# Performance work log

Measured on AMD Instinct MI355X. Metric: run time of the kernel, lower is better.

## Reference

```python
import jax, jax.numpy as jnp
import numpy as np

B, N = 8192, 4096
OUT_DIM = 32


def setup_inputs() -> dict:
    key = jax.random.key(0)
    k_rr, k_drop, k_w1, k_b1, k_w2, k_b2 = jax.random.split(key, 6)
    rr = jax.random.uniform(k_rr, (B, N), dtype=jnp.float32, minval=0.4, maxval=1.4)
    drop = jax.random.uniform(k_drop, (B, N)) < 0.3
    rr = jnp.where(drop, 0.0, rr)
    # projection MLP params (Linear(6,16) -> ReLU -> Dropout(eval: identity) -> Linear(16,32))
    w1 = jax.random.normal(k_w1, (6, 16), dtype=jnp.float32) * (1.0 / np.sqrt(6))
    b1 = jax.random.normal(k_b1, (16,), dtype=jnp.float32) * 0.01
    w2 = jax.random.normal(k_w2, (16, OUT_DIM), dtype=jnp.float32) * (1.0 / np.sqrt(16))
    b2 = jax.random.normal(k_b2, (OUT_DIM,), dtype=jnp.float32) * 0.01
    return {"rr_intervals": rr, "w1": w1, "b1": b1, "w2": w2, "b2": b2}


def _hrv_features(rr):
    # rr: (B, N) float32, zero-padded. Faithful to the per-row torch loop, vectorized.
    dt = rr.dtype
    mask = rr > 0                                   # (B, N)
    cnt = jnp.sum(mask, axis=1)                     # (B,) int
    cntf = cnt.astype(dt)
    # masked mean / unbiased std (torch.std default ddof=1)
    denom_m = jnp.maximum(cntf, 1.0)
    mean_rr = jnp.sum(jnp.where(mask, rr, 0.0), axis=1) / denom_m
    dev = jnp.where(mask, rr - mean_rr[:, None], 0.0)
    var = jnp.sum(dev * dev, axis=1) / jnp.maximum(cntf - 1.0, 1.0)
    sdnn = jnp.sqrt(var)
    # compact valid entries to the front (stable -> preserves order), so diffs
    # match torch.diff(rr[rr > 0])
    order = jnp.argsort(jnp.logical_not(mask), axis=1, stable=True)  # (B, N)
    compact = jnp.take_along_axis(rr, order, axis=1)                  # (B, N)
    diffs = compact[:, 1:] - compact[:, :-1]                          # (B, N-1)
    dmask = jnp.arange(N - 1)[None, :] < (cnt - 1)[:, None]           # valid diffs
    ndiff = jnp.maximum(cntf - 1.0, 1.0)
    rmssd = jnp.sqrt(jnp.sum(jnp.where(dmask, diffs * diffs, 0.0), axis=1) / ndiff)
    nn50 = jnp.sum(((jnp.abs(diffs) > 0.05) & dmask).astype(dt), axis=1)
    pnn50 = nn50 / ndiff
    hr = 60.0 / jnp.maximum(mean_rr, 1e-12)
    cv = sdnn / jnp.maximum(mean_rr, 1e-12)
    feats = jnp.stack([mean_rr, sdnn, rmssd, pnn50, hr, cv], axis=1)  # (B, 6)
    feats = jnp.where((cnt > 1)[:, None], feats, 0.0)
    # per-column batch normalization, applied only where column max > 0
    col_max = jnp.max(feats, axis=0)
    col_mean = jnp.mean(feats, axis=0)
    col_std = jnp.std(feats, axis=0, ddof=1)
    normed = (feats - col_mean[None, :]) / (col_std[None, :] + 1e-8)
    feats = jnp.where((col_max > 0)[None, :], normed, feats)
    return feats


def reference(rr_intervals, w1, b1, w2, b2):
    feats = _hrv_features(rr_intervals)                 # (B, 6)
    h = jax.nn.relu(feats @ w1 + b1)                    # (B, 16); dropout in eval = identity
    return h @ w2 + b2                                  # (B, OUT_DIM)
```

## Files before the change

### kernel.cpp

```cpp
#include <hip/hip_runtime.h>
#include <math.h>

#define BATCH 8192
#define NLEN 4096

__global__ __launch_bounds__(256) void hrv_feats_kernel(
    const float* __restrict__ rr, float* __restrict__ feats) {
    const int lane = threadIdx.x & 63;
    const int wid = threadIdx.x >> 6;
    const int row = blockIdx.x * 4 + wid;
    const float* r = rr + (size_t)row * NLEN + lane * 64;

    double dsum = 0.0, dsumsq = 0.0, dsumd2 = 0.0;
    int cnt = 0, nn50 = 0, has = 0;
    float first = 0.f, last = 0.f;

    float x[32];
    float4* xv = reinterpret_cast<float4*>(x);
    const float4* rv = reinterpret_cast<const float4*>(r);

#pragma unroll
    for (int half = 0; half < 2; ++half) {
#pragma unroll
        for (int i = 0; i < 8; ++i) xv[i] = rv[half * 8 + i];
#pragma unroll
        for (int c = 0; c < 2; ++c) {
            float s = 0.f, s2 = 0.f, d2 = 0.f;
#pragma unroll
            for (int i = 0; i < 16; ++i) {
                float v = x[c * 16 + i];
                if (v > 0.f) {
                    s += v;
                    s2 += v * v;
                    ++cnt;
                    if (has) {
                        float d = v - last;
                        d2 += d * d;
                        nn50 += (fabsf(d) > 0.05f) ? 1 : 0;
                    } else {
                        first = v;
                        has = 1;
                    }
                    last = v;
                }
            }
            dsum += s;
            dsumsq += s2;
            dsumd2 += d2;
        }
    }

    unsigned long long m = __ballot(has != 0);
    unsigned long long pm = (lane == 0) ? 0ull : (m & ((1ull << lane) - 1ull));
    int j = 63 - __clzll(pm | 1ull);
    float lastj = __shfl(last, j, 64);
    if (has && pm) {
        float d = first - lastj;
        dsumd2 += (double)(d * d);
        nn50 += (fabsf(d) > 0.05f) ? 1 : 0;
    }

#pragma unroll
    for (int off = 32; off; off >>= 1) {
        dsum += __shfl_down(dsum, off, 64);
        dsumsq += __shfl_down(dsumsq, off, 64);
        dsumd2 += __shfl_down(dsumd2, off, 64);
        cnt += __shfl_down(cnt, off, 64);
        nn50 += __shfl_down(nn50, off, 64);
    }

    if (lane == 0) {
        const float cntf = (float)cnt;
        const float denom_m = fmaxf(cntf, 1.f);
        const float mean = (float)(dsum / (double)denom_m);
        const float varsum = (float)(dsumsq - (double)cnt * (double)mean * (double)mean);
        const float denom_v = fmaxf(cntf - 1.f, 1.f);
        const float sdnn = sqrtf(fmaxf(varsum / denom_v, 0.f));
        const float rmssd = sqrtf(fmaxf((float)(dsumd2 / (double)denom_v), 0.f));
        const float pnn50 = (float)nn50 / denom_v;
        const float hr = 60.f / fmaxf(mean, 1e-12f);
        const float cv = sdnn / fmaxf(mean, 1e-12f);
        float f0 = mean, f1 = sdnn, f2 = rmssd, f3 = pnn50, f4 = hr, f5 = cv;
        if (cnt <= 1) { f0 = f1 = f2 = f3 = f4 = f5 = 0.f; }
        float* o = feats + row * 6;
        o[0] = f0; o[1] = f1; o[2] = f2;
        o[3] = f3; o[4] = f4; o[5] = f5;
    }
}

__global__ __launch_bounds__(256) void stats_mlp_kernel(
    const float* __restrict__ feats,
    const float* __restrict__ w1, const float* __restrict__ b1,
    const float* __restrict__ w2, const float* __restrict__ b2,
    float* __restrict__ out) {
    __shared__ double sh_s[4][6], sh_s2[4][6];
    __shared__ float sh_m[4][6];
    __shared__ float sh_stats[18];

    const int t = threadIdx.x;
    double s[6] = {0, 0, 0, 0, 0, 0};
    double s2[6] = {0, 0, 0, 0, 0, 0};
    float mx[6] = {-INFINITY, -INFINITY, -INFINITY, -INFINITY, -INFINITY, -INFINITY};

#pragma unroll 4
    for (int i = t; i < BATCH; i += 256) {
        const float* fp = feats + i * 6;
#pragma unroll
        for (int c = 0; c < 6; ++c) {
            float f = fp[c];
            s[c] += (double)f;
            s2[c] += (double)f * (double)f;
            mx[c] = fmaxf(mx[c], f);
        }
    }
#pragma unroll
    for (int off = 32; off; off >>= 1) {
#pragma unroll
        for (int c = 0; c < 6; ++c) {
            s[c] += __shfl_down(s[c], off, 64);
            s2[c] += __shfl_down(s2[c], off, 64);
            mx[c] = fmaxf(mx[c], __shfl_down(mx[c], off, 64));
        }
    }
    if ((t & 63) == 0) {
        const int w = t >> 6;
#pragma unroll
        for (int c = 0; c < 6; ++c) {
            sh_s[w][c] = s[c];
            sh_s2[w][c] = s2[c];
            sh_m[w][c] = mx[c];
        }
    }
    __syncthreads();
    if (t < 6) {
        double S = 0, S2 = 0;
        float M = -INFINITY;
        for (int w = 0; w < 4; ++w) {
            S += sh_s[w][t];
            S2 += sh_s2[w][t];
            M = fmaxf(M, sh_m[w][t]);
        }
        const double meanb = S / (double)BATCH;
        double var = (S2 - (double)BATCH * meanb * meanb) / (double)(BATCH - 1);
        if (var < 0.0) var = 0.0;
        sh_stats[t] = (float)meanb;
        sh_stats[6 + t] = (float)sqrt(var);
        sh_stats[12 + t] = M;
    }
    __syncthreads();

    const int row = blockIdx.x * 256 + t;
    const float* fp = feats + row * 6;
    float f[6];
#pragma unroll
    for (int c = 0; c < 6; ++c) {
        float v = fp[c];
        if (sh_stats[12 + c] > 0.f) v = (v - sh_stats[c]) / (sh_stats[6 + c] + 1e-8f);
        f[c] = v;
    }
    float h[16];
#pragma unroll
    for (int j = 0; j < 16; ++j) {
        float a = b1[j];
#pragma unroll
        for (int c = 0; c < 6; ++c) a = fmaf(f[c], w1[c * 16 + j], a);
        h[j] = fmaxf(a, 0.f);
    }
    float o[32];
#pragma unroll
    for (int k = 0; k < 32; ++k) o[k] = b2[k];
#pragma unroll
    for (int j = 0; j < 16; ++j) {
        const float hj = h[j];
#pragma unroll
        for (int k = 0; k < 32; ++k) o[k] = fmaf(hj, w2[j * 32 + k], o[k]);
    }
    float4* ov = reinterpret_cast<float4*>(out + (size_t)row * 32);
    const float4* op = reinterpret_cast<const float4*>(o);
#pragma unroll
    for (int i = 0; i < 8; ++i) ov[i] = op[i];
}

extern "C" void kernel_launch(void* const* d_in, const int* in_sizes, int n_in,
                              void* d_out, int out_size, void* d_ws, size_t ws_size,
                              hipStream_t stream) {
    const float* rr = (const float*)d_in[0];
    const float* w1 = (const float*)d_in[1];
    const float* b1 = (const float*)d_in[2];
    const float* w2 = (const float*)d_in[3];
    const float* b2 = (const float*)d_in[4];
    float* out = (float*)d_out;
    float* feats = (float*)d_ws;

    hrv_feats_kernel<<<BATCH / 4, 256, 0, stream>>>(rr, feats);
    stats_mlp_kernel<<<BATCH / 256, 256, 0, stream>>>(feats, w1, b1, w2, b2, out);
}
```

Measured before the change: 41.59 us.

## Coalesce row loads with lane-interleaved float4 chunks and per-chunk ballot stitching

Each lane now reads a float4 at stride 256 floats, so a wavefront's loads cover contiguous memory instead of each lane reading its own 64-float span. Because consecutive valid elements now cross lanes at every chunk, the code does a ballot and shuffle per chunk to find the previous valid value and carries a running last value across chunks. This targets poor load coalescing on the bandwidth-bound pass over the input. In exchange it adds 16 ballot/shuffle rounds per row, which costs extra ALU and cross-lane work.

```diff
diff --git a/kernel.cpp b/kernel.cpp
--- a/kernel.cpp
+++ b/kernel.cpp
@@ -9,26 +9,29 @@
     const int lane = threadIdx.x & 63;
     const int wid = threadIdx.x >> 6;
     const int row = blockIdx.x * 4 + wid;
-    const float* r = rr + (size_t)row * NLEN + lane * 64;
+    const float* rbase = rr + (size_t)row * NLEN + lane * 4;
 
     double dsum = 0.0, dsumsq = 0.0, dsumd2 = 0.0;
-    int cnt = 0, nn50 = 0, has = 0;
-    float first = 0.f, last = 0.f;
-
-    float x[32];
-    float4* xv = reinterpret_cast<float4*>(x);
-    const float4* rv = reinterpret_cast<const float4*>(r);
+    int cnt = 0, nn50 = 0;
+    float run_last = 0.f;
+    int run_has = 0;
 
 #pragma unroll
     for (int half = 0; half < 2; ++half) {
-#pragma unroll
-        for (int i = 0; i < 8; ++i) xv[i] = rv[half * 8 + i];
-#pragma unroll
-        for (int c = 0; c < 2; ++c) {
-            float s = 0.f, s2 = 0.f, d2 = 0.f;
-#pragma unroll
-            for (int i = 0; i < 16; ++i) {
-                float v = x[c * 16 + i];
+        float4 v4[8];
+#pragma unroll
+        for (int ii = 0; ii < 8; ++ii)
+            v4[ii] = *reinterpret_cast<const float4*>(rbase + (half * 8 + ii) * 256);
+
+        float s = 0.f, s2 = 0.f, d2 = 0.f;
+#pragma unroll
+        for (int ii = 0; ii < 8; ++ii) {
+            const float x[4] = {v4[ii].x, v4[ii].y, v4[ii].z, v4[ii].w};
+            float first = 0.f, last = 0.f;
+            int has = 0;
+#pragma unroll
+            for (int k = 0; k < 4; ++k) {
+                float v = x[k];
                 if (v > 0.f) {
                     s += v;
                     s2 += v * v;
@@ -44,20 +47,26 @@
                     last = v;
                 }
             }
-            dsum += s;
-            dsumsq += s2;
-            dsumd2 += d2;
-        }
-    }
-
-    unsigned long long m = __ballot(has != 0);
-    unsigned long long pm = (lane == 0) ? 0ull : (m & ((1ull << lane) - 1ull));
-    int j = 63 - __clzll(pm | 1ull);
-    float lastj = __shfl(last, j, 64);
-    if (has && pm) {
-        float d = first - lastj;
-        dsumd2 += (double)(d * d);
-        nn50 += (fabsf(d) > 0.05f) ? 1 : 0;
+            unsigned long long m = __ballot(has != 0);
+            unsigned long long pm = m & ((1ull << lane) - 1ull);
+            int j = 63 - __clzll(pm | 1ull);
+            float lastj = __shfl(last, j, 64);
+            float pred = pm ? lastj : run_last;
+            int pred_has = pm ? 1 : run_has;
+            if (has && pred_has) {
+                float d = first - pred;
+                d2 += d * d;
+                nn50 += (fabsf(d) > 0.05f) ? 1 : 0;
+            }
+            if (m) {
+                int jm = 63 - __clzll(m);
+                run_last = __shfl(last, jm, 64);
+                run_has = 1;
+            }
+        }
+        dsum += s;
+        dsumsq += s2;
+        dsumd2 += d2;
     }
 
 #pragma unroll
```

New measurement: 42.79 us. 1.03x slower.

## Branchless HRV accumulation, column-major feature layout, vectorized stats reads

Applied to the files above, without the earlier changes.

Replaces the per-element data-dependent branches in the feature kernel with predicated selects and FMAs. This relies on invalid entries being exactly zero, so adding them to the sums changes nothing. The reduction now uses xor shuffles so every lane holds the totals, and six lanes each write one feature into a column-major (6 x BATCH) workspace. The stats kernel reads each column with float4 loads and reads the features coalesced in the MLP stage, which removes strided 6-float row accesses. The risk is extra ALU work per element where the branchy version could skip invalid values.

```diff
diff --git a/kernel.cpp b/kernel.cpp
--- a/kernel.cpp
+++ b/kernel.cpp
@@ -12,8 +12,9 @@
     const float* r = rr + (size_t)row * NLEN + lane * 64;
 
     double dsum = 0.0, dsumsq = 0.0, dsumd2 = 0.0;
-    int cnt = 0, nn50 = 0, has = 0;
-    float first = 0.f, last = 0.f;
+    int cnt = 0, nn50 = 0;
+    float prev = 0.f, first = 0.f;
+    bool has = false;
 
     float x[32];
     float4* xv = reinterpret_cast<float4*>(x);
@@ -28,21 +29,18 @@
             float s = 0.f, s2 = 0.f, d2 = 0.f;
 #pragma unroll
             for (int i = 0; i < 16; ++i) {
-                float v = x[c * 16 + i];
-                if (v > 0.f) {
-                    s += v;
-                    s2 += v * v;
-                    ++cnt;
-                    if (has) {
-                        float d = v - last;
-                        d2 += d * d;
-                        nn50 += (fabsf(d) > 0.05f) ? 1 : 0;
-                    } else {
-                        first = v;
-                        has = 1;
-                    }
-                    last = v;
-                }
+                const float v = x[c * 16 + i];
+                const bool valid = v > 0.f;
+                s += v;
+                s2 = fmaf(v, v, s2);
+                cnt += valid ? 1 : 0;
+                const float d = v - prev;
+                const float dm = (valid && has) ? d : 0.f;
+                d2 = fmaf(dm, dm, d2);
+                nn50 += (fabsf(dm) > 0.05f) ? 1 : 0;
+                first = (valid && !has) ? v : first;
+                prev = valid ? v : prev;
+                has = has || valid;
             }
             dsum += s;
             dsumsq += s2;
@@ -50,10 +48,10 @@
         }
     }
 
-    unsigned long long m = __ballot(has != 0);
-    unsigned long long pm = (lane == 0) ? 0ull : (m & ((1ull << lane) - 1ull));
+    unsigned long long m = __ballot(has);
+    unsigned long long pm = m & ((1ull << lane) - 1ull);
     int j = 63 - __clzll(pm | 1ull);
-    float lastj = __shfl(last, j, 64);
+    float lastj = __shfl(prev, j, 64);
     if (has && pm) {
         float d = first - lastj;
         dsumd2 += (double)(d * d);
@@ -62,30 +60,32 @@
 
 #pragma unroll
     for (int off = 32; off; off >>= 1) {
-        dsum += __shfl_down(dsum, off, 64);
-        dsumsq += __shfl_down(dsumsq, off, 64);
-        dsumd2 += __shfl_down(dsumd2, off, 64);
-        cnt += __shfl_down(cnt, off, 64);
-        nn50 += __shfl_down(nn50, off, 64);
-    }
-
-    if (lane == 0) {
-        const float cntf = (float)cnt;
-        const float denom_m = fmaxf(cntf, 1.f);
-        const float mean = (float)(dsum / (double)denom_m);
-        const float varsum = (float)(dsumsq - (double)cnt * (double)mean * (double)mean);
-        const float denom_v = fmaxf(cntf - 1.f, 1.f);
-        const float sdnn = sqrtf(fmaxf(varsum / denom_v, 0.f));
-        const float rmssd = sqrtf(fmaxf((float)(dsumd2 / (double)denom_v), 0.f));
-        const float pnn50 = (float)nn50 / denom_v;
-        const float hr = 60.f / fmaxf(mean, 1e-12f);
-        const float cv = sdnn / fmaxf(mean, 1e-12f);
-        float f0 = mean, f1 = sdnn, f2 = rmssd, f3 = pnn50, f4 = hr, f5 = cv;
-        if (cnt <= 1) { f0 = f1 = f2 = f3 = f4 = f5 = 0.f; }
-        float* o = feats + row * 6;
-        o[0] = f0; o[1] = f1; o[2] = f2;
-        o[3] = f3; o[4] = f4; o[5] = f5;
-    }
+        dsum += __shfl_xor(dsum, off, 64);
+        dsumsq += __shfl_xor(dsumsq, off, 64);
+        dsumd2 += __shfl_xor(dsumd2, off, 64);
+        cnt += __shfl_xor(cnt, off, 64);
+        nn50 += __shfl_xor(nn50, off, 64);
+    }
+
+    const float cntf = (float)cnt;
+    const float denom_m = fmaxf(cntf, 1.f);
+    const float mean = (float)(dsum / (double)denom_m);
+    const float varsum = (float)(dsumsq - (double)cnt * (double)mean * (double)mean);
+    const float denom_v = fmaxf(cntf - 1.f, 1.f);
+    const float sdnn = sqrtf(fmaxf(varsum / denom_v, 0.f));
+    const float rmssd = sqrtf(fmaxf((float)(dsumd2 / (double)denom_v), 0.f));
+    const float pnn50 = (float)nn50 / denom_v;
+    const float hr = 60.f / fmaxf(mean, 1e-12f);
+    const float cv = sdnn / fmaxf(mean, 1e-12f);
+
+    float val = mean;
+    val = (lane == 1) ? sdnn : val;
+    val = (lane == 2) ? rmssd : val;
+    val = (lane == 3) ? pnn50 : val;
+    val = (lane == 4) ? hr : val;
+    val = (lane == 5) ? cv : val;
+    if (cnt <= 1) val = 0.f;
+    if (lane < 6) feats[lane * BATCH + row] = val;
 }
 
 __global__ __launch_bounds__(256) void stats_mlp_kernel(
@@ -98,19 +98,24 @@
     __shared__ float sh_stats[18];
 
     const int t = threadIdx.x;
-    double s[6] = {0, 0, 0, 0, 0, 0};
-    double s2[6] = {0, 0, 0, 0, 0, 0};
-    float mx[6] = {-INFINITY, -INFINITY, -INFINITY, -INFINITY, -INFINITY, -INFINITY};
-
-#pragma unroll 4
-    for (int i = t; i < BATCH; i += 256) {
-        const float* fp = feats + i * 6;
-#pragma unroll
-        for (int c = 0; c < 6; ++c) {
-            float f = fp[c];
-            s[c] += (double)f;
-            s2[c] += (double)f * (double)f;
-            mx[c] = fmaxf(mx[c], f);
+    double s[6], s2[6];
+    float mx[6];
+#pragma unroll
+    for (int c = 0; c < 6; ++c) { s[c] = 0.0; s2[c] = 0.0; mx[c] = -INFINITY; }
+
+#pragma unroll
+    for (int c = 0; c < 6; ++c) {
+        const float4* col = reinterpret_cast<const float4*>(feats + c * BATCH);
+#pragma unroll
+        for (int it = 0; it < BATCH / 4 / 256; ++it) {
+            float4 f4 = col[t + it * 256];
+            const float f[4] = {f4.x, f4.y, f4.z, f4.w};
+#pragma unroll
+            for (int k = 0; k < 4; ++k) {
+                s[c] += (double)f[k];
+                s2[c] += (double)f[k] * (double)f[k];
+                mx[c] = fmaxf(mx[c], f[k]);
+            }
         }
     }
 #pragma unroll
@@ -150,11 +155,10 @@
     __syncthreads();
 
     const int row = blockIdx.x * 256 + t;
-    const float* fp = feats + row * 6;
     float f[6];
 #pragma unroll
     for (int c = 0; c < 6; ++c) {
-        float v = fp[c];
+        float v = feats[c * BATCH + row];
         if (sh_stats[12 + c] > 0.f) v = (v - sh_stats[c]) / (sh_stats[6 + c] + 1e-8f);
         f[c] = v;
     }
```

After: 42.54 us. +2.3%, slower.
